# Performance work log

Measured on AMD Instinct MI355X. Metric: run time of the kernel, lower is better.

## Reference

```python
import jax, jax.numpy as jnp
import numpy as np

S = 128          # shared sequence length of v/q/a/k
D = 512          # model dim
H = 8            # n_heads
W = D // H       # head width (becomes the v/q/a einsum axes)
NUM = S // 8     # num_v = num_q = num_a = num_k
SCALE = float(np.sqrt(H))  # source divides by sqrt(a.size(-1)) == sqrt(n_heads)


def _heads(x):
    # split_last(x,(H,-1)).transpose(1,2) on a 2D (S,D) tensor -> (S, W, H)
    return x.reshape(S, H, W).transpose(0, 2, 1)


def setup_inputs() -> dict:
    key = jax.random.key(0)
    ks = jax.random.split(key, 24)
    d = {}
    for i, n in enumerate(['v', 'q', 'a', 'k']):
        d[n] = jax.random.normal(ks[i], (S, D), jnp.float32)
    for n in ['v_mask', 'q_mask', 'a_mask', 'k_mask']:
        d[n] = jnp.ones((S,), jnp.bool_)
    wnames = ['Wv', 'Wq', 'Wa', 'Wk', 'Wvo', 'Wqo', 'Wao', 'Wko']
    bnames = ['bv', 'bq', 'ba', 'bk', 'bvo', 'bqo', 'bao', 'bko']
    for i, (wn, bn) in enumerate(zip(wnames, bnames)):
        d[wn] = jax.random.normal(ks[4 + 2 * i], (D, D), jnp.float32) / np.sqrt(D)
        d[bn] = jax.random.normal(ks[5 + 2 * i], (D,), jnp.float32) * 0.01
    return d


def reference(v, q, a, k, v_mask, q_mask, a_mask, k_mask,
              Wv, bv, Wq, bq, Wa, ba, Wk, bk,
              Wvo, bvo, Wqo, bqo, Wao, bao, Wko, bko):
    # input projections (torch Linear: x @ W.T + b)
    vp = v @ Wv.T + bv
    qp = q @ Wq.T + bq
    ap = a @ Wa.T + ba
    kp = k @ Wk.T + bk
    # output projections are applied to the already-projected tensors
    vo = vp @ Wvo.T + bvo
    qo = qp @ Wqo.T + bqo
    ao = ap @ Wao.T + bao
    ko = kp @ Wko.T + bko
    tv, tq, ta, tk = map(_heads, (vp, qp, ap, kp))      # (S, W, H)
    tvo, tqo, tao, tko = map(_heads, (vo, qo, ao, ko))  # (S, W, H)
    # trilinear scores: in source labels b=1, h=S, v/q/a in W, w=H
    att = jnp.einsum('sic,sjc,slc->sijl', tv, tq, ta) / SCALE   # (S, W, W, W)
    att1 = jnp.einsum('sic,sjc,slc->sijl', tv, tq, tk) / SCALE  # (S, W, W, W)
    # joint softmax over the flat num_v*num_q*num_a axis (flat memory reshape,
    # exactly like torch .view); dropout p=0.0 -> identity
    scores = jax.nn.softmax(att.reshape(-1, H, NUM * NUM * NUM), axis=-1)
    scores = scores.reshape(-1, H, NUM, NUM, NUM)  # stored as self.scores in torch
    # output contractions use the UNNORMALIZED att1 (as in the source)
    v_res = jnp.einsum('sijl,sic->isc', att1, tvo).reshape(1, W, S * H)
    q_res = jnp.einsum('sijl,sjc->jsc', att1, tqo).reshape(1, W, S * H)
    a_res = jnp.einsum('sijl,slc->lsc', att1, tao).reshape(1, W, S * H)
    k_res = tko[None].reshape(1, S, W * H)
    return (v_res, q_res, a_res, k_res, scores)
```

## Files before the change

kernel.cpp:

```cpp
#include <hip/hip_runtime.h>
#include <hip/hip_bf16.h>

#define INV_SCALE 0.35355339059327373f

struct Proj4Args {
  const float* x[4];
  const float* w[4];
  const float* b[4];
  float* y[4];
};

__global__ __launch_bounds__(256) void proj4_kernel(Proj4Args A) {
  const int blk = blockIdx.x;
  const int p = blk >> 6;
  const int s0 = (blk & 63) * 2;
  const int t = threadIdx.x;
  __shared__ float xL[2][512];
  {
    const float2* xr = (const float2*)A.x[p];
    float2 f0 = xr[s0 * 256 + t];
    float2 f1 = xr[(s0 + 1) * 256 + t];
    xL[0][2 * t] = f0.x; xL[0][2 * t + 1] = f0.y;
    xL[1][2 * t] = f1.x; xL[1][2 * t + 1] = f1.y;
  }
  __syncthreads();
  const float b0 = A.b[p][t];
  const float b1 = A.b[p][t + 256];
  float a00 = b0, a01 = b1, a10 = b0, a11 = b1;
  const float* Wp = A.w[p];
  const float4* wr0 = (const float4*)(Wp + t * 512);
  const float4* wr1 = (const float4*)(Wp + (t + 256) * 512);
#pragma unroll 8
  for (int k4 = 0; k4 < 128; ++k4) {
    float4 wa = wr0[k4];
    float4 wb = wr1[k4];
    float wv[4] = {wa.x, wa.y, wa.z, wa.w};
    float vv[4] = {wb.x, wb.y, wb.z, wb.w};
    const float* xp0 = &xL[0][k4 * 4];
    const float* xp1 = &xL[1][k4 * 4];
#pragma unroll
    for (int x = 0; x < 4; ++x) {
      float xa = xp0[x], xb = xp1[x];
      a00 = fmaf(wv[x], xa, a00);
      a01 = fmaf(vv[x], xa, a01);
      a10 = fmaf(wv[x], xb, a10);
      a11 = fmaf(vv[x], xb, a11);
    }
  }
  float* yp = A.y[p];
  yp[s0 * 512 + t] = a00;
  yp[s0 * 512 + t + 256] = a01;
  yp[(s0 + 1) * 512 + t] = a10;
  yp[(s0 + 1) * 512 + t + 256] = a11;
}

__global__ __launch_bounds__(256) void post_kernel(
    const float* __restrict__ vp, const float* __restrict__ qp,
    const float* __restrict__ kp, const float* __restrict__ vo,
    const float* __restrict__ qo, const float* __restrict__ ao,
    const float* __restrict__ ko, float* __restrict__ out) {
  const int s = blockIdx.x;
  const int t = threadIdx.x;
  const int wid = t >> 6;
  const int ln = t & 63;
  __shared__ float Ssum[3][8];
  const float* srcs[3] = {vp, qp, kp};
#pragma unroll
  for (int tt = 0; tt < 3; ++tt) {
    const float* r = srcs[tt] + s * 512;
    float a = r[wid * 64 + ln];
    float b = r[256 + wid * 64 + ln];
#pragma unroll
    for (int o = 32; o; o >>= 1) {
      a += __shfl_xor(a, o);
      b += __shfl_xor(b, o);
    }
    if (ln == 0) { Ssum[tt][wid] = a; Ssum[tt][wid + 4] = b; }
  }
  __syncthreads();
  if (wid == 3) {
    float tmp[8];
#pragma unroll
    for (int h = 0; h < 8; ++h)
      tmp[h] = ko[s * 512 + h * 64 + ln];
    float4* pp = reinterpret_cast<float4*>(out + 196608 + (s * 64 + ln) * 8);
    pp[0] = make_float4(tmp[0], tmp[1], tmp[2], tmp[3]);
    pp[1] = make_float4(tmp[4], tmp[5], tmp[6], tmp[7]);
  } else {
    const float* base = (wid == 0) ? vp : (wid == 1) ? qp : kp;
    const float* obase = (wid == 0) ? vo : (wid == 1) ? qo : ao;
    const int c0 = (wid == 0) ? 1 : 0;
    const int c1 = (wid == 2) ? 1 : 2;
    float A1 = 0.f;
#pragma unroll
    for (int c = 0; c < 8; ++c)
      A1 += base[s * 512 + c * 64 + ln] * (Ssum[c0][c] * Ssum[c1][c]);
    A1 *= INV_SCALE;
    float tmp[8];
#pragma unroll
    for (int c = 0; c < 8; ++c)
      tmp[c] = obase[s * 512 + c * 64 + ln] * A1;
    float4* pp = reinterpret_cast<float4*>(out + wid * 65536 + (ln * 128 + s) * 8);
    pp[0] = make_float4(tmp[0], tmp[1], tmp[2], tmp[3]);
    pp[1] = make_float4(tmp[4], tmp[5], tmp[6], tmp[7]);
  }
}

__global__ __launch_bounds__(256) void scores_kernel(
    const float* __restrict__ vp, const float* __restrict__ qp,
    const float* __restrict__ ap, float* __restrict__ out) {
  const int b = blockIdx.x;
  const int s = b >> 4;
  const int i0 = (b & 15) * 4;
  const int t = threadIdx.x;
  __shared__ float tqL[512];
  __shared__ float taL[512];
  __shared__ float uL[32];
  __shared__ float redM[4][4];
  __shared__ float redS[4][4];
  {
    const float* qr = qp + s * 512;
    const float* ar = ap + s * 512;
    tqL[t] = qr[t]; tqL[t + 256] = qr[t + 256];
    taL[t] = ar[t]; taL[t + 256] = ar[t + 256];
    if (t < 32) {
      int ii = t >> 3, c = t & 7;
      uL[t] = vp[s * 512 + c * 64 + i0 + ii] * INV_SCALE;
    }
  }
  __syncthreads();
  const int j0 = t >> 3;
  const int l0 = (t & 7) * 8;
  float acc[4][16];
#pragma unroll
  for (int ii = 0; ii < 4; ++ii)
#pragma unroll
    for (int x = 0; x < 16; ++x) acc[ii][x] = 0.f;
#pragma unroll
  for (int c = 0; c < 8; ++c) {
    float t0 = tqL[c * 64 + j0];
    float t1 = tqL[c * 64 + j0 + 32];
    float4 A0 = *reinterpret_cast<const float4*>(&taL[c * 64 + l0]);
    float4 A1v = *reinterpret_cast<const float4*>(&taL[c * 64 + l0 + 4]);
    float ta8[8] = {A0.x, A0.y, A0.z, A0.w, A1v.x, A1v.y, A1v.z, A1v.w};
#pragma unroll
    for (int ii = 0; ii < 4; ++ii) {
      float uv = uL[ii * 8 + c];
      float m0 = uv * t0;
      float m1 = uv * t1;
#pragma unroll
      for (int x = 0; x < 8; ++x) {
        acc[ii][x] = fmaf(m0, ta8[x], acc[ii][x]);
        acc[ii][8 + x] = fmaf(m1, ta8[x], acc[ii][8 + x]);
      }
    }
  }
  const int wid = t >> 6, ln = t & 63;
#pragma unroll
  for (int ii = 0; ii < 4; ++ii) {
    float m = acc[ii][0];
#pragma unroll
    for (int x = 1; x < 16; ++x) m = fmaxf(m, acc[ii][x]);
#pragma unroll
    for (int o = 32; o; o >>= 1) m = fmaxf(m, __shfl_xor(m, o));
    if (ln == 0) redM[ii][wid] = m;
  }
  __syncthreads();
#pragma unroll
  for (int ii = 0; ii < 4; ++ii) {
    float mf = fmaxf(fmaxf(redM[ii][0], redM[ii][1]),
                     fmaxf(redM[ii][2], redM[ii][3]));
    float sl = 0.f;
#pragma unroll
    for (int x = 0; x < 16; ++x) {
      float e = __expf(acc[ii][x] - mf);
      acc[ii][x] = e;
      sl += e;
    }
#pragma unroll
    for (int o = 32; o; o >>= 1) sl += __shfl_xor(sl, o);
    if (ln == 0) redS[ii][wid] = sl;
  }
  __syncthreads();
  const long sbase = 262144L + (long)s * 262144 + (long)i0 * 4096;
#pragma unroll
  for (int ii = 0; ii < 4; ++ii) {
    float tot = (redS[ii][0] + redS[ii][1]) + (redS[ii][2] + redS[ii][3]);
    float sc = 1.0f / tot;
#pragma unroll
    for (int jj = 0; jj < 2; ++jj) {
      float4* pp = reinterpret_cast<float4*>(
          out + sbase + ii * 4096 + (j0 + jj * 32) * 64 + l0);
      pp[0] = make_float4(acc[ii][jj * 8 + 0] * sc, acc[ii][jj * 8 + 1] * sc,
                          acc[ii][jj * 8 + 2] * sc, acc[ii][jj * 8 + 3] * sc);
      pp[1] = make_float4(acc[ii][jj * 8 + 4] * sc, acc[ii][jj * 8 + 5] * sc,
                          acc[ii][jj * 8 + 6] * sc, acc[ii][jj * 8 + 7] * sc);
    }
  }
}

extern "C" void kernel_launch(void* const* d_in, const int* in_sizes, int n_in,
                              void* d_out, int out_size, void* d_ws, size_t ws_size,
                              hipStream_t stream) {
  int wb = 8;
  if (n_in >= 5 && in_sizes[4] == 262144) wb = 4;
  const float* W[8];
  const float* B[8];
  for (int i = 0; i < 8; ++i) {
    W[i] = (const float*)d_in[wb + 2 * i];
    B[i] = (const float*)d_in[wb + 2 * i + 1];
  }
  float* ws = (float*)d_ws;
  float* vp = ws;
  float* qp = ws + 65536;
  float* ap = ws + 131072;
  float* kp = ws + 196608;
  float* vo = ws + 262144;
  float* qo = ws + 327680;
  float* ao = ws + 393216;
  float* ko = ws + 458752;
  float* out = (float*)d_out;

  Proj4Args a1;
  for (int i = 0; i < 4; ++i) {
    a1.x[i] = (const float*)d_in[i];
    a1.w[i] = W[i];
    a1.b[i] = B[i];
  }
  a1.y[0] = vp; a1.y[1] = qp; a1.y[2] = ap; a1.y[3] = kp;
  hipLaunchKernelGGL(proj4_kernel, dim3(256), dim3(256), 0, stream, a1);

  Proj4Args a2;
  a2.x[0] = vp; a2.x[1] = qp; a2.x[2] = ap; a2.x[3] = kp;
  for (int i = 0; i < 4; ++i) {
    a2.w[i] = W[4 + i];
    a2.b[i] = B[4 + i];
  }
  a2.y[0] = vo; a2.y[1] = qo; a2.y[2] = ao; a2.y[3] = ko;
  hipLaunchKernelGGL(proj4_kernel, dim3(256), dim3(256), 0, stream, a2);

  hipLaunchKernelGGL(post_kernel, dim3(128), dim3(256), 0, stream,
                     vp, qp, kp, vo, qo, ao, ko, out);
  hipLaunchKernelGGL(scores_kernel, dim3(2048), dim3(256), 0, stream,
                     vp, qp, ap, out);
}
```

Baseline: 270.2 us.

## Tile projection GEMM by output columns with shared weight slab and transposed X tiles

Each projection block now owns 8 output columns for all 128 rows. It stages the 8x512 weight slab in shared memory and streams X through a padded transposed shared tile, prefetching the next tile into registers. Previously each block handled 2 rows and read every full weight row from global memory, so W was re-read 64 times. The new layout reads W once per block, at the cost of reading all of X per block, 16 sync-separated chunks, and heavier shared-memory traffic.

```diff
diff --git a/kernel.cpp b/kernel.cpp
--- a/kernel.cpp
+++ b/kernel.cpp
@@ -13,45 +13,67 @@
 __global__ __launch_bounds__(256) void proj4_kernel(Proj4Args A) {
   const int blk = blockIdx.x;
   const int p = blk >> 6;
-  const int s0 = (blk & 63) * 2;
+  const int dbase = (blk & 63) * 8;
   const int t = threadIdx.x;
-  __shared__ float xL[2][512];
+  const int s = t & 127;
+  const int h = t >> 7;
+  __shared__ float WL[8 * 512];
+  __shared__ float XT[32][129];
   {
-    const float2* xr = (const float2*)A.x[p];
-    float2 f0 = xr[s0 * 256 + t];
-    float2 f1 = xr[(s0 + 1) * 256 + t];
-    xL[0][2 * t] = f0.x; xL[0][2 * t + 1] = f0.y;
-    xL[1][2 * t] = f1.x; xL[1][2 * t + 1] = f1.y;
-  }
-  __syncthreads();
-  const float b0 = A.b[p][t];
-  const float b1 = A.b[p][t + 256];
-  float a00 = b0, a01 = b1, a10 = b0, a11 = b1;
-  const float* Wp = A.w[p];
-  const float4* wr0 = (const float4*)(Wp + t * 512);
-  const float4* wr1 = (const float4*)(Wp + (t + 256) * 512);
-#pragma unroll 8
-  for (int k4 = 0; k4 < 128; ++k4) {
-    float4 wa = wr0[k4];
-    float4 wb = wr1[k4];
-    float wv[4] = {wa.x, wa.y, wa.z, wa.w};
-    float vv[4] = {wb.x, wb.y, wb.z, wb.w};
-    const float* xp0 = &xL[0][k4 * 4];
-    const float* xp1 = &xL[1][k4 * 4];
-#pragma unroll
-    for (int x = 0; x < 4; ++x) {
-      float xa = xp0[x], xb = xp1[x];
-      a00 = fmaf(wv[x], xa, a00);
-      a01 = fmaf(vv[x], xa, a01);
-      a10 = fmaf(wv[x], xb, a10);
-      a11 = fmaf(vv[x], xb, a11);
-    }
-  }
-  float* yp = A.y[p];
-  yp[s0 * 512 + t] = a00;
-  yp[s0 * 512 + t + 256] = a01;
-  yp[(s0 + 1) * 512 + t] = a10;
-  yp[(s0 + 1) * 512 + t + 256] = a11;
+    const float4* wg = (const float4*)(A.w[p] + dbase * 512);
+    float4* wl4 = (float4*)WL;
+#pragma unroll
+    for (int r = 0; r < 4; ++r) wl4[t + r * 256] = wg[t + r * 256];
+  }
+  const float* xg = A.x[p];
+  const int row = t >> 3;
+  const int col = t & 7;
+  float acc[4] = {0.f, 0.f, 0.f, 0.f};
+  float4 pre[4];
+#pragma unroll
+  for (int r = 0; r < 4; ++r)
+    pre[r] = ((const float4*)(xg + (row + r * 32) * 512))[col];
+  for (int c = 0; c < 16; ++c) {
+    __syncthreads();
+#pragma unroll
+    for (int r = 0; r < 4; ++r) {
+      float4 f = pre[r];
+      int rr = row + r * 32;
+      XT[col * 4 + 0][rr] = f.x;
+      XT[col * 4 + 1][rr] = f.y;
+      XT[col * 4 + 2][rr] = f.z;
+      XT[col * 4 + 3][rr] = f.w;
+    }
+    __syncthreads();
+    if (c + 1 < 16) {
+#pragma unroll
+      for (int r = 0; r < 4; ++r)
+        pre[r] = ((const float4*)(xg + (row + r * 32) * 512))[(c + 1) * 8 + col];
+    }
+#pragma unroll
+    for (int k4 = 0; k4 < 8; ++k4) {
+      float xv0 = XT[k4 * 4 + 0][s];
+      float xv1 = XT[k4 * 4 + 1][s];
+      float xv2 = XT[k4 * 4 + 2][s];
+      float xv3 = XT[k4 * 4 + 3][s];
+#pragma unroll
+      for (int di = 0; di < 4; ++di) {
+        const float4 wv =
+            *(const float4*)&WL[(h * 4 + di) * 512 + c * 32 + k4 * 4];
+        acc[di] = fmaf(wv.x, xv0, acc[di]);
+        acc[di] = fmaf(wv.y, xv1, acc[di]);
+        acc[di] = fmaf(wv.z, xv2, acc[di]);
+        acc[di] = fmaf(wv.w, xv3, acc[di]);
+      }
+    }
+  }
+  const float* bp = A.b[p];
+  float4 o;
+  o.x = acc[0] + bp[dbase + h * 4 + 0];
+  o.y = acc[1] + bp[dbase + h * 4 + 1];
+  o.z = acc[2] + bp[dbase + h * 4 + 2];
+  o.w = acc[3] + bp[dbase + h * 4 + 3];
+  *(float4*)(A.y[p] + s * 512 + dbase + h * 4) = o;
 }
 
 __global__ __launch_bounds__(256) void post_kernel(
```

Measured after the change: 245.2 us. -9.3%, faster.
